# Optimization experiments

Measured on AMD Instinct MI355X. Metric: run time of the kernel, lower is better.

The kernel has to match this reference:

```python
import jax, jax.numpy as jnp
import numpy as np

N = 100000   # nodes
E = 1600000  # edges (avg degree 16)
F_IN, F_HID, F_OUT = 64, 64, 16


def setup_inputs() -> dict:
    key = jax.random.key(0)
    ks = jax.random.split(key, 10)
    features = jax.random.normal(ks[0], (N, F_IN), dtype=jnp.float32)
    src = jax.random.randint(ks[1], (E,), 0, N, dtype=jnp.int32)
    dst = jax.random.randint(ks[2], (E,), 0, N, dtype=jnp.int32)
    # Xavier-uniform weights, zero bias (matches nn.init in the module)
    def xavier(k, fan_in, fan_out):
        lim = np.sqrt(6.0 / (fan_in + fan_out))
        return jax.random.uniform(k, (fan_in, fan_out), jnp.float32, -lim, lim)
    return {
        "features": features,
        "W1": xavier(ks[3], F_IN, F_HID), "b1": jnp.zeros((F_HID,), jnp.float32),
        "W2": xavier(ks[4], F_HID, F_HID), "b2": jnp.zeros((F_HID,), jnp.float32),
        "W3": xavier(ks[5], F_HID, F_OUT), "b3": jnp.zeros((F_OUT,), jnp.float32),
        "src": src, "dst": dst,
    }


def pairnorm_scs(x):
    # PairNorm 'PN-SCS', scale=1
    col_mean = x.mean(axis=0)                                    # [F]
    rownorm = jnp.sqrt(1e-6 + jnp.sum(x * x, axis=1, keepdims=True))  # [N,1]
    return x / rownorm - col_mean


def graph_conv(h, src, dst, W, b):
    # copy_u('h','m') + sum reduce over edges, plus self-loop
    agg = jax.ops.segment_sum(h[src], dst, num_segments=N) + h   # [N,F]
    return agg @ W + b


def reference(features, W1, b1, W2, b2, W3, b3, src, dst):
    h = features
    for W, b in ((W1, b1), (W2, b2)):
        h = pairnorm_scs(h)
        h = jax.nn.relu(graph_conv(h, src, dst, W, b))
        # dropout p=0.0 -> identity
    return graph_conv(h, src, dst, W3, b3)
```

## Files before the change

### kernel.cpp

```cpp
#include <hip/hip_runtime.h>


#define NHB 128

__device__ __forceinline__ unsigned short f2bf(float f) {
  unsigned u = __builtin_bit_cast(unsigned, f);
  u += 0x7FFFu + ((u >> 16) & 1u);
  return (unsigned short)(u >> 16);
}
__device__ __forceinline__ float bf2f(unsigned short h) {
  return __builtin_bit_cast(float, ((unsigned)h) << 16);
}
__device__ __forceinline__ float rlane(float v, int k) {
  return __builtin_bit_cast(
      float, __builtin_amdgcn_readlane(__builtin_bit_cast(int, v), k));
}

__global__ __launch_bounds__(256) void prelude_kernel(
    const int* __restrict__ dst, int* __restrict__ cntA, int E,
    const float* __restrict__ x, float* __restrict__ cs, int n4) {
  __shared__ int lc[NHB];
  __shared__ float lds[16][64];
  const int t = threadIdx.x;
  if (t < NHB) lc[t] = 0;
  __syncthreads();
  const int stride = gridDim.x * blockDim.x;
  for (int e = blockIdx.x * blockDim.x + t; e < E; e += stride)
    atomicAdd(&lc[__builtin_nontemporal_load(&dst[e]) >> 10], 1);

  float s0 = 0.f, s1 = 0.f, s2 = 0.f, s3 = 0.f;
  for (int i = blockIdx.x * blockDim.x + t; i < n4; i += stride) {
    float4 v = ((const float4*)x)[i];
    s0 += v.x; s1 += v.y; s2 += v.z; s3 += v.w;
  }
  const int r = t >> 4;
  const int cq = (t & 15) * 4;
  lds[r][cq + 0] = s0; lds[r][cq + 1] = s1; lds[r][cq + 2] = s2; lds[r][cq + 3] = s3;
  __syncthreads();
  if (t < NHB && lc[t]) atomicAdd(&cntA[t], lc[t]);
  if (t < 64) {
    float tot = 0.f;
    #pragma unroll
    for (int rr = 0; rr < 16; ++rr) tot += lds[rr][t];
    unsafeAtomicAdd(&cs[t], tot);
  }
}

__global__ void colsum_kernel(const float* __restrict__ x, float* __restrict__ cs,
                              int n4) {
  __shared__ float lds[16][64];
  float s0 = 0.f, s1 = 0.f, s2 = 0.f, s3 = 0.f;
  const int t = threadIdx.x;
  const int stride = gridDim.x * blockDim.x;
  for (int i = blockIdx.x * blockDim.x + t; i < n4; i += stride) {
    float4 v = ((const float4*)x)[i];
    s0 += v.x; s1 += v.y; s2 += v.z; s3 += v.w;
  }
  const int r = t >> 4;
  const int cq = (t & 15) * 4;
  lds[r][cq + 0] = s0; lds[r][cq + 1] = s1; lds[r][cq + 2] = s2; lds[r][cq + 3] = s3;
  __syncthreads();
  if (t < 64) {
    float tot = 0.f;
    #pragma unroll
    for (int rr = 0; rr < 16; ++rr) tot += lds[rr][t];
    unsafeAtomicAdd(&cs[t], tot);
  }
}

__global__ __launch_bounds__(256) void matnorm_kernel(
    const float* x, const float* __restrict__ W,
    const float* __restrict__ cs, unsigned short* __restrict__ z,
    int N, float invN) {
  const int lane = threadIdx.x & 63;
  const int wid  = blockIdx.x * (blockDim.x >> 6) + (threadIdx.x >> 6);
  const int nw   = gridDim.x * (blockDim.x >> 6);

  float w[64];
  float cm0 = 0.f, cm1 = 0.f, cm2 = 0.f, cm3 = 0.f;
  #pragma unroll
  for (int k = 0; k < 64; k += 4) {
    w[k + 0] = W[(k + 0) * 64 + lane];
    w[k + 1] = W[(k + 1) * 64 + lane];
    w[k + 2] = W[(k + 2) * 64 + lane];
    w[k + 3] = W[(k + 3) * 64 + lane];
    cm0 = fmaf(cs[k + 0], w[k + 0], cm0);
    cm1 = fmaf(cs[k + 1], w[k + 1], cm1);
    cm2 = fmaf(cs[k + 2], w[k + 2], cm2);
    cm3 = fmaf(cs[k + 3], w[k + 3], cm3);
  }
  const float cm = ((cm0 + cm1) + (cm2 + cm3)) * invN;

  for (int row = wid; row < N; row += nw) {
    const float xv = x[(size_t)row * 64 + lane];
    float ss = xv * xv;
    #pragma unroll
    for (int m = 1; m < 64; m <<= 1) ss += __shfl_xor(ss, m, 64);
    const float rinv = 1.0f / sqrtf(1e-6f + ss);
    float a0 = 0.f, a1 = 0.f, a2 = 0.f, a3 = 0.f;
    #pragma unroll
    for (int k = 0; k < 64; k += 4) {
      a0 = fmaf(rlane(xv, k + 0), w[k + 0], a0);
      a1 = fmaf(rlane(xv, k + 1), w[k + 1], a1);
      a2 = fmaf(rlane(xv, k + 2), w[k + 2], a2);
      a3 = fmaf(rlane(xv, k + 3), w[k + 3], a3);
    }
    const float acc = (a0 + a1) + (a2 + a3);
    z[(size_t)row * 64 + lane] = f2bf(acc * rinv - cm);
  }
}


__global__ void scanA_kernel(const int* __restrict__ cntA,
                             int* __restrict__ baseA, int* __restrict__ curA,
                             int NHI) {
  if (threadIdx.x == 0) {
    int acc = 0;
    for (int p = 0; p < NHI; ++p) { baseA[p] = acc; curA[p] = acc; acc += cntA[p]; }
    baseA[NHI] = acc;
  }
}

#define TILE 2048
#define CAPA 48
__global__ __launch_bounds__(256) void scatterA_kernel(
    const int* __restrict__ src, const int* __restrict__ dst,
    int* __restrict__ curA, unsigned* __restrict__ ppack, int E) {
  __shared__ unsigned lpk[NHB][CAPA];
  __shared__ int lcnt[NHB], lbase[NHB];
  const int t = threadIdx.x;
  if (t < NHB) lcnt[t] = 0;
  __syncthreads();
  const int ntiles = (E + TILE - 1) / TILE;
  for (int tile = blockIdx.x; tile < ntiles; tile += gridDim.x) {
    const int base = tile * TILE;
    #pragma unroll
    for (int j = 0; j < TILE / 256; ++j) {
      const int e = base + j * 256 + t;
      if (e < E) {
        const int d = __builtin_nontemporal_load(&dst[e]);
        const int s = __builtin_nontemporal_load(&src[e]);
        const unsigned pw = ((unsigned)s << 10) | ((unsigned)d & 1023u);
        const int p = d >> 10;
        const int slot = atomicAdd(&lcnt[p], 1);
        if (slot < CAPA) lpk[p][slot] = pw;
        else ppack[atomicAdd(&curA[p], 1)] = pw;
      }
    }
    __syncthreads();
    if (t < NHB) {
      int c = lcnt[t]; if (c > CAPA) c = CAPA;
      lbase[t] = c ? atomicAdd(&curA[t], c) : 0;
      lcnt[t] = c;
    }
    __syncthreads();
    for (int p = 0; p < NHB; ++p) {
      const int c = lcnt[p];
      if (t < c) ppack[lbase[p] + t] = lpk[p][t];
    }
    __syncthreads();
    if (t < NHB) lcnt[t] = 0;
    __syncthreads();
  }
}

__global__ __launch_bounds__(1024) void fillsort_kernel(
    const unsigned* __restrict__ ppack, const int* __restrict__ baseA,
    int* __restrict__ rowstart, int* __restrict__ csr, int N, int E) {
  __shared__ int hist[1024];
  __shared__ int bs[1024];
  const int t = threadIdx.x;
  const int h = blockIdx.x;
  const int nlo = h << 10;
  const int elo = baseA[h], ehi = baseA[h + 1];

  hist[t] = 0;
  __syncthreads();

  int e = elo + t;
  for (; e + 3 * 1024 < ehi; e += 4 * 1024) {
    const unsigned p0 = ppack[e], p1 = ppack[e + 1024],
                   p2 = ppack[e + 2048], p3 = ppack[e + 3072];
    atomicAdd(&hist[p0 & 1023u], 1); atomicAdd(&hist[p1 & 1023u], 1);
    atomicAdd(&hist[p2 & 1023u], 1); atomicAdd(&hist[p3 & 1023u], 1);
  }
  for (; e < ehi; e += 1024) atomicAdd(&hist[ppack[e] & 1023u], 1);
  __syncthreads();

  const int c = hist[t];
  bs[t] = c;
  __syncthreads();
  for (int off = 1; off < 1024; off <<= 1) {
    const int v = (t >= off) ? bs[t - off] : 0;
    __syncthreads();
    bs[t] += v;
    __syncthreads();
  }
  const int excl = bs[t] - c;

  hist[t] = excl;
  const int n0 = nlo + t;
  if (n0 < N) rowstart[n0] = elo + excl;
  if (h == 0 && t == 0) rowstart[N] = E;
  __syncthreads();

  e = elo + t;
  for (; e + 3 * 1024 < ehi; e += 4 * 1024) {
    const unsigned p0 = ppack[e],        p1 = ppack[e + 1024];
    const unsigned p2 = ppack[e + 2048], p3 = ppack[e + 3072];
    csr[elo + atomicAdd(&hist[p0 & 1023u], 1)] = (int)(p0 >> 10);
    csr[elo + atomicAdd(&hist[p1 & 1023u], 1)] = (int)(p1 >> 10);
    csr[elo + atomicAdd(&hist[p2 & 1023u], 1)] = (int)(p2 >> 10);
    csr[elo + atomicAdd(&hist[p3 & 1023u], 1)] = (int)(p3 >> 10);
  }
  for (; e < ehi; e += 1024) {
    const unsigned p = ppack[e];
    csr[elo + atomicAdd(&hist[p & 1023u], 1)] = (int)(p >> 10);
  }
}

__global__ __launch_bounds__(256) void gather64_kernel(
    const unsigned short* __restrict__ z, const float* __restrict__ b,
    const int* __restrict__ rowstart, const int* __restrict__ csr,
    float* __restrict__ agg, int N) {
  const int lane = threadIdx.x & 63;
  int node = blockIdx.x * (blockDim.x >> 6) + (threadIdx.x >> 6);
  if (node >= N) return;
  node = __builtin_amdgcn_readfirstlane(node);
  const int start = rowstart[node];
  const int end   = rowstart[node + 1];
  const unsigned short hs = z[(size_t)node * 64 + lane];
  float a0 = 0.f, a1 = 0.f, a2 = 0.f, a3 = 0.f;
  int e = start;
  for (; e + 16 <= end; e += 16) {
    unsigned short h[16];
    #pragma unroll
    for (int j = 0; j < 16; ++j) h[j] = z[(size_t)csr[e + j] * 64 + lane];
    #pragma unroll
    for (int j = 0; j < 16; j += 4) {
      a0 += bf2f(h[j + 0]); a1 += bf2f(h[j + 1]);
      a2 += bf2f(h[j + 2]); a3 += bf2f(h[j + 3]);
    }
  }
  for (; e + 4 <= end; e += 4) {
    unsigned short h[4];
    #pragma unroll
    for (int j = 0; j < 4; ++j) h[j] = z[(size_t)csr[e + j] * 64 + lane];
    a0 += bf2f(h[0]); a1 += bf2f(h[1]); a2 += bf2f(h[2]); a3 += bf2f(h[3]);
  }
  for (; e < end; ++e) a0 += bf2f(z[(size_t)csr[e] * 64 + lane]);
  const float sum = (a0 + a1) + (a2 + a3);
  agg[(size_t)node * 64 + lane] = fmaxf(bf2f(hs) + b[lane] + sum, 0.f);
}

__global__ __launch_bounds__(256) void gather_l2_kernel(
    const unsigned short* __restrict__ z2, const float* __restrict__ b2,
    const float* __restrict__ W3, const int* __restrict__ rowstart,
    const int* __restrict__ csr, unsigned short* __restrict__ z3, int N) {
  const int lane = threadIdx.x & 63;
  int node = blockIdx.x * (blockDim.x >> 6) + (threadIdx.x >> 6);
  if (node >= N) return;
  node = __builtin_amdgcn_readfirstlane(node);
  float4 w4[4];
  #pragma unroll
  for (int q = 0; q < 4; ++q)
    w4[q] = ((const float4*)(W3 + lane * 16))[q];

  const int start = rowstart[node];
  const int end   = rowstart[node + 1];
  const unsigned short hs = z2[(size_t)node * 64 + lane];
  float a0 = 0.f, a1 = 0.f, a2 = 0.f, a3 = 0.f;
  int e = start;
  for (; e + 16 <= end; e += 16) {
    unsigned short h[16];
    #pragma unroll
    for (int j = 0; j < 16; ++j) h[j] = z2[(size_t)csr[e + j] * 64 + lane];
    #pragma unroll
    for (int j = 0; j < 16; j += 4) {
      a0 += bf2f(h[j + 0]); a1 += bf2f(h[j + 1]);
      a2 += bf2f(h[j + 2]); a3 += bf2f(h[j + 3]);
    }
  }
  for (; e + 4 <= end; e += 4) {
    unsigned short h[4];
    #pragma unroll
    for (int j = 0; j < 4; ++j) h[j] = z2[(size_t)csr[e + j] * 64 + lane];
    a0 += bf2f(h[0]); a1 += bf2f(h[1]); a2 += bf2f(h[2]); a3 += bf2f(h[3]);
  }
  for (; e < end; ++e) a0 += bf2f(z2[(size_t)csr[e] * 64 + lane]);
  const float sum = (a0 + a1) + (a2 + a3);
  const float o = fmaxf(bf2f(hs) + b2[lane] + sum, 0.f);

  float p[16];
  #pragma unroll
  for (int q = 0; q < 4; ++q) {
    p[4 * q + 0] = o * w4[q].x;
    p[4 * q + 1] = o * w4[q].y;
    p[4 * q + 2] = o * w4[q].z;
    p[4 * q + 3] = o * w4[q].w;
  }
  {
    const bool up = (lane & 1);
    #pragma unroll
    for (int m = 0; m < 8; ++m) {
      const float mine = up ? p[m + 8] : p[m];
      const float give = up ? p[m] : p[m + 8];
      p[m] = mine + __shfl_xor(give, 1, 64);
    }
  }
  {
    const bool up = (lane & 2);
    #pragma unroll
    for (int m = 0; m < 4; ++m) {
      const float mine = up ? p[m + 4] : p[m];
      const float give = up ? p[m] : p[m + 4];
      p[m] = mine + __shfl_xor(give, 2, 64);
    }
  }
  {
    const bool up = (lane & 4);
    #pragma unroll
    for (int m = 0; m < 2; ++m) {
      const float mine = up ? p[m + 2] : p[m];
      const float give = up ? p[m] : p[m + 2];
      p[m] = mine + __shfl_xor(give, 4, 64);
    }
  }
  {
    const bool up = (lane & 8);
    const float mine = up ? p[1] : p[0];
    const float give = up ? p[0] : p[1];
    p[0] = mine + __shfl_xor(give, 8, 64);
  }
  p[0] += __shfl_xor(p[0], 16, 64);
  p[0] += __shfl_xor(p[0], 32, 64);

  if (lane < 16) {
    const int j = ((lane & 1) << 3) | ((lane & 2) << 1) |
                  ((lane & 4) >> 1) | ((lane & 8) >> 3);
    z3[(size_t)node * 16 + j] = f2bf(p[0]);
  }
}

__global__ __launch_bounds__(256) void gather16_kernel(
    const unsigned short* __restrict__ z3, const float* __restrict__ b3,
    const int* __restrict__ rowstart, const int* __restrict__ csr,
    float* __restrict__ out, int N) {
  const int lane = threadIdx.x & 63;
  const int f = lane & 15;
  const int g = lane >> 4;
  int node = blockIdx.x * (blockDim.x >> 6) + (threadIdx.x >> 6);
  if (node >= N) return;
  node = __builtin_amdgcn_readfirstlane(node);
  const int start = rowstart[node];
  const int end   = rowstart[node + 1];
  float acc0 = 0.f, acc1 = 0.f;
  int e = start + g;
  for (; e + 4 < end; e += 8) {
    acc0 += bf2f(z3[(size_t)csr[e] * 16 + f]);
    acc1 += bf2f(z3[(size_t)csr[e + 4] * 16 + f]);
  }
  if (e < end) acc0 += bf2f(z3[(size_t)csr[e] * 16 + f]);
  float acc = acc0 + acc1;
  acc += __shfl_xor(acc, 16, 64);
  acc += __shfl_xor(acc, 32, 64);
  if (lane < 16)
    out[(size_t)node * 16 + f] = bf2f(z3[(size_t)node * 16 + f]) + b3[f] + acc;
}

extern "C" void kernel_launch(void* const* d_in, const int* in_sizes, int n_in,
                              void* d_out, int out_size, void* d_ws, size_t ws_size,
                              hipStream_t stream) {
  const float* feat = (const float*)d_in[0];
  const float* W1 = (const float*)d_in[1];
  const float* b1 = (const float*)d_in[2];
  const float* W2 = (const float*)d_in[3];
  const float* b2 = (const float*)d_in[4];
  const float* W3 = (const float*)d_in[5];
  const float* b3 = (const float*)d_in[6];
  const int* src = (const int*)d_in[7];
  const int* dst = (const int*)d_in[8];
  const int N = in_sizes[0] / 64;
  const int E = in_sizes[7];
  float* out = (float*)d_out;

  float* B            = (float*)d_ws;
  unsigned short* zb  = (unsigned short*)(B + (size_t)N * 64);
  unsigned short* z3b = zb + (size_t)N * 64;
  int* cntA  = (int*)(z3b + (size_t)N * 16);
  float* cs1 = (float*)(cntA + NHB);
  float* cs2 = cs1 + 64;
  int* baseA    = (int*)(cs2 + 64);
  int* curA     = baseA + NHB + 1;
  int* rowstart = curA + NHB;
  int* csr      = rowstart + N + 1;
  unsigned* ppack = (unsigned*)zb;

  const int NHI = (N + 1023) >> 10;
  const int node_blocks = (N + 3) / 4;
  const float invN = 1.0f / (float)N;

  hipMemsetAsync(cntA, 0, (NHB + 128) * sizeof(int), stream);
  prelude_kernel<<<512, 256, 0, stream>>>(dst, cntA, E, feat, cs1, N * 16);
  scanA_kernel<<<1, 64, 0, stream>>>(cntA, baseA, curA, NHI);
  scatterA_kernel<<<512, 256, 0, stream>>>(src, dst, curA, ppack, E);
  fillsort_kernel<<<NHI, 1024, 0, stream>>>(ppack, baseA, rowstart, csr, N, E);

  matnorm_kernel<<<1024, 256, 0, stream>>>(feat, W1, cs1, zb, N, invN);
  gather64_kernel<<<node_blocks, 256, 0, stream>>>(zb, b1, rowstart, csr, B, N);

  colsum_kernel<<<512, 256, 0, stream>>>(B, cs2, N * 16);
  matnorm_kernel<<<1024, 256, 0, stream>>>(B, W2, cs2, zb, N, invN);
  gather_l2_kernel<<<node_blocks, 256, 0, stream>>>(zb, b2, W3, rowstart, csr,
                                                    z3b, N);

  gather16_kernel<<<node_blocks, 256, 0, stream>>>(z3b, b3, rowstart, csr, out, N);
}
```

Before: 402.5 us.

## Process two nodes per wavefront in 64-wide gathers with shuffled CSR indices

The two 64-feature gather kernels now give each wavefront a pair of adjacent nodes instead of one. The combined neighbor index list (up to 64 entries) is loaded once with a single coalesced read and broadcast with shuffles, replacing per-edge scalar index loads. Neighbor rows are fetched in full batches of 16 across the node boundary to keep more loads in flight. Extra branching and per-edge tails handle the split point, and the grid is halved, which may reduce the number of waves available to hide latency.

```diff
diff --git a/kernel.cpp b/kernel.cpp
--- a/kernel.cpp
+++ b/kernel.cpp
@@ -224,73 +224,68 @@
     const int* __restrict__ rowstart, const int* __restrict__ csr,
     float* __restrict__ agg, int N) {
   const int lane = threadIdx.x & 63;
-  int node = blockIdx.x * (blockDim.x >> 6) + (threadIdx.x >> 6);
-  if (node >= N) return;
-  node = __builtin_amdgcn_readfirstlane(node);
-  const int start = rowstart[node];
-  const int end   = rowstart[node + 1];
-  const unsigned short hs = z[(size_t)node * 64 + lane];
-  float a0 = 0.f, a1 = 0.f, a2 = 0.f, a3 = 0.f;
-  int e = start;
-  for (; e + 16 <= end; e += 16) {
+  int pair = blockIdx.x * (blockDim.x >> 6) + (threadIdx.x >> 6);
+  const int n0 = pair << 1;
+  if (n0 >= N) return;
+  pair = __builtin_amdgcn_readfirstlane(pair);
+  const int has2 = (n0 + 1 < N);
+  const int s0  = rowstart[n0];
+  const int mid = rowstart[n0 + 1];
+  const int e1  = has2 ? rowstart[n0 + 2] : mid;
+  const int ntot = e1 - s0;
+  const int nA   = mid - s0;
+
+  const int cidx = (lane < ntot) ? csr[s0 + lane] : 0;
+
+  const unsigned short hs0 = z[(size_t)n0 * 64 + lane];
+  const unsigned short hs1 = has2 ? z[(size_t)(n0 + 1) * 64 + lane] : (unsigned short)0;
+
+  float aA0 = 0.f, aA1 = 0.f, aA2 = 0.f, aA3 = 0.f;
+  float aB0 = 0.f, aB1 = 0.f, aB2 = 0.f, aB3 = 0.f;
+  const int lim = ntot < 64 ? ntot : 64;
+  for (int j0 = 0; j0 < lim; j0 += 16) {
+    int id[16];
+    #pragma unroll
+    for (int k = 0; k < 16; ++k) id[k] = __shfl(cidx, j0 + k, 64);
     unsigned short h[16];
     #pragma unroll
-    for (int j = 0; j < 16; ++j) h[j] = z[(size_t)csr[e + j] * 64 + lane];
-    #pragma unroll
-    for (int j = 0; j < 16; j += 4) {
-      a0 += bf2f(h[j + 0]); a1 += bf2f(h[j + 1]);
-      a2 += bf2f(h[j + 2]); a3 += bf2f(h[j + 3]);
-    }
-  }
-  for (; e + 4 <= end; e += 4) {
-    unsigned short h[4];
-    #pragma unroll
-    for (int j = 0; j < 4; ++j) h[j] = z[(size_t)csr[e + j] * 64 + lane];
-    a0 += bf2f(h[0]); a1 += bf2f(h[1]); a2 += bf2f(h[2]); a3 += bf2f(h[3]);
-  }
-  for (; e < end; ++e) a0 += bf2f(z[(size_t)csr[e] * 64 + lane]);
-  const float sum = (a0 + a1) + (a2 + a3);
-  agg[(size_t)node * 64 + lane] = fmaxf(bf2f(hs) + b[lane] + sum, 0.f);
-}
-
-__global__ __launch_bounds__(256) void gather_l2_kernel(
-    const unsigned short* __restrict__ z2, const float* __restrict__ b2,
-    const float* __restrict__ W3, const int* __restrict__ rowstart,
-    const int* __restrict__ csr, unsigned short* __restrict__ z3, int N) {
-  const int lane = threadIdx.x & 63;
-  int node = blockIdx.x * (blockDim.x >> 6) + (threadIdx.x >> 6);
-  if (node >= N) return;
-  node = __builtin_amdgcn_readfirstlane(node);
-  float4 w4[4];
-  #pragma unroll
-  for (int q = 0; q < 4; ++q)
-    w4[q] = ((const float4*)(W3 + lane * 16))[q];
-
-  const int start = rowstart[node];
-  const int end   = rowstart[node + 1];
-  const unsigned short hs = z2[(size_t)node * 64 + lane];
-  float a0 = 0.f, a1 = 0.f, a2 = 0.f, a3 = 0.f;
-  int e = start;
-  for (; e + 16 <= end; e += 16) {
-    unsigned short h[16];
-    #pragma unroll
-    for (int j = 0; j < 16; ++j) h[j] = z2[(size_t)csr[e + j] * 64 + lane];
-    #pragma unroll
-    for (int j = 0; j < 16; j += 4) {
-      a0 += bf2f(h[j + 0]); a1 += bf2f(h[j + 1]);
-      a2 += bf2f(h[j + 2]); a3 += bf2f(h[j + 3]);
-    }
-  }
-  for (; e + 4 <= end; e += 4) {
-    unsigned short h[4];
-    #pragma unroll
-    for (int j = 0; j < 4; ++j) h[j] = z2[(size_t)csr[e + j] * 64 + lane];
-    a0 += bf2f(h[0]); a1 += bf2f(h[1]); a2 += bf2f(h[2]); a3 += bf2f(h[3]);
-  }
-  for (; e < end; ++e) a0 += bf2f(z2[(size_t)csr[e] * 64 + lane]);
-  const float sum = (a0 + a1) + (a2 + a3);
-  const float o = fmaxf(bf2f(hs) + b2[lane] + sum, 0.f);
-
+    for (int k = 0; k < 16; ++k) h[k] = z[(size_t)id[k] * 64 + lane];
+    if (j0 + 16 <= nA) {
+      #pragma unroll
+      for (int k = 0; k < 16; k += 4) {
+        aA0 += bf2f(h[k + 0]); aA1 += bf2f(h[k + 1]);
+        aA2 += bf2f(h[k + 2]); aA3 += bf2f(h[k + 3]);
+      }
+    } else if (j0 >= nA && j0 + 16 <= lim) {
+      #pragma unroll
+      for (int k = 0; k < 16; k += 4) {
+        aB0 += bf2f(h[k + 0]); aB1 += bf2f(h[k + 1]);
+        aB2 += bf2f(h[k + 2]); aB3 += bf2f(h[k + 3]);
+      }
+    } else {
+      #pragma unroll
+      for (int k = 0; k < 16; ++k) {
+        const int j = j0 + k;
+        const float v = (j < lim) ? bf2f(h[k]) : 0.f;
+        if (j < nA) aA0 += v; else aB0 += v;
+      }
+    }
+  }
+  for (int e = s0 + 64; e < e1; ++e) {
+    const float v = bf2f(z[(size_t)csr[e] * 64 + lane]);
+    if (e < mid) aA0 += v; else aB0 += v;
+  }
+
+  const float sumA = (aA0 + aA1) + (aA2 + aA3);
+  agg[(size_t)n0 * 64 + lane] = fmaxf(bf2f(hs0) + b[lane] + sumA, 0.f);
+  if (has2) {
+    const float sumB = (aB0 + aB1) + (aB2 + aB3);
+    agg[(size_t)(n0 + 1) * 64 + lane] = fmaxf(bf2f(hs1) + b[lane] + sumB, 0.f);
+  }
+}
+
+__device__ __forceinline__ void w3_matvec_store(
+    float o, const float4* w4, int lane, unsigned short* __restrict__ z3row) {
   float p[16];
   #pragma unroll
   for (int q = 0; q < 4; ++q) {
@@ -334,11 +329,82 @@
   }
   p[0] += __shfl_xor(p[0], 16, 64);
   p[0] += __shfl_xor(p[0], 32, 64);
-
   if (lane < 16) {
     const int j = ((lane & 1) << 3) | ((lane & 2) << 1) |
                   ((lane & 4) >> 1) | ((lane & 8) >> 3);
-    z3[(size_t)node * 16 + j] = f2bf(p[0]);
+    z3row[j] = f2bf(p[0]);
+  }
+}
+
+__global__ __launch_bounds__(256) void gather_l2_kernel(
+    const unsigned short* __restrict__ z2, const float* __restrict__ b2,
+    const float* __restrict__ W3, const int* __restrict__ rowstart,
+    const int* __restrict__ csr, unsigned short* __restrict__ z3, int N) {
+  const int lane = threadIdx.x & 63;
+  int pair = blockIdx.x * (blockDim.x >> 6) + (threadIdx.x >> 6);
+  const int n0 = pair << 1;
+  if (n0 >= N) return;
+  pair = __builtin_amdgcn_readfirstlane(pair);
+  float4 w4[4];
+  #pragma unroll
+  for (int q = 0; q < 4; ++q)
+    w4[q] = ((const float4*)(W3 + lane * 16))[q];
+
+  const int has2 = (n0 + 1 < N);
+  const int s0  = rowstart[n0];
+  const int mid = rowstart[n0 + 1];
+  const int e1  = has2 ? rowstart[n0 + 2] : mid;
+  const int ntot = e1 - s0;
+  const int nA   = mid - s0;
+
+  const int cidx = (lane < ntot) ? csr[s0 + lane] : 0;
+
+  const unsigned short hs0 = z2[(size_t)n0 * 64 + lane];
+  const unsigned short hs1 = has2 ? z2[(size_t)(n0 + 1) * 64 + lane] : (unsigned short)0;
+
+  float aA0 = 0.f, aA1 = 0.f, aA2 = 0.f, aA3 = 0.f;
+  float aB0 = 0.f, aB1 = 0.f, aB2 = 0.f, aB3 = 0.f;
+  const int lim = ntot < 64 ? ntot : 64;
+  for (int j0 = 0; j0 < lim; j0 += 16) {
+    int id[16];
+    #pragma unroll
+    for (int k = 0; k < 16; ++k) id[k] = __shfl(cidx, j0 + k, 64);
+    unsigned short h[16];
+    #pragma unroll
+    for (int k = 0; k < 16; ++k) h[k] = z2[(size_t)id[k] * 64 + lane];
+    if (j0 + 16 <= nA) {
+      #pragma unroll
+      for (int k = 0; k < 16; k += 4) {
+        aA0 += bf2f(h[k + 0]); aA1 += bf2f(h[k + 1]);
+        aA2 += bf2f(h[k + 2]); aA3 += bf2f(h[k + 3]);
+      }
+    } else if (j0 >= nA && j0 + 16 <= lim) {
+      #pragma unroll
+      for (int k = 0; k < 16; k += 4) {
+        aB0 += bf2f(h[k + 0]); aB1 += bf2f(h[k + 1]);
+        aB2 += bf2f(h[k + 2]); aB3 += bf2f(h[k + 3]);
+      }
+    } else {
+      #pragma unroll
+      for (int k = 0; k < 16; ++k) {
+        const int j = j0 + k;
+        const float v = (j < lim) ? bf2f(h[k]) : 0.f;
+        if (j < nA) aA0 += v; else aB0 += v;
+      }
+    }
+  }
+  for (int e = s0 + 64; e < e1; ++e) {
+    const float v = bf2f(z2[(size_t)csr[e] * 64 + lane]);
+    if (e < mid) aA0 += v; else aB0 += v;
+  }
+
+  const float sumA = (aA0 + aA1) + (aA2 + aA3);
+  const float oA = fmaxf(bf2f(hs0) + b2[lane] + sumA, 0.f);
+  w3_matvec_store(oA, w4, lane, z3 + (size_t)n0 * 16);
+  if (has2) {
+    const float sumB = (aB0 + aB1) + (aB2 + aB3);
+    const float oB = fmaxf(bf2f(hs1) + b2[lane] + sumB, 0.f);
+    w3_matvec_store(oB, w4, lane, z3 + (size_t)(n0 + 1) * 16);
   }
 }
 
@@ -398,6 +464,8 @@
 
   const int NHI = (N + 1023) >> 10;
   const int node_blocks = (N + 3) / 4;
+  const int npairs = (N + 1) / 2;
+  const int pair_blocks = (npairs + 3) / 4;
   const float invN = 1.0f / (float)N;
 
   hipMemsetAsync(cntA, 0, (NHB + 128) * sizeof(int), stream);
@@ -407,11 +475,11 @@
   fillsort_kernel<<<NHI, 1024, 0, stream>>>(ppack, baseA, rowstart, csr, N, E);
 
   matnorm_kernel<<<1024, 256, 0, stream>>>(feat, W1, cs1, zb, N, invN);
-  gather64_kernel<<<node_blocks, 256, 0, stream>>>(zb, b1, rowstart, csr, B, N);
+  gather64_kernel<<<pair_blocks, 256, 0, stream>>>(zb, b1, rowstart, csr, B, N);
 
   colsum_kernel<<<512, 256, 0, stream>>>(B, cs2, N * 16);
   matnorm_kernel<<<1024, 256, 0, stream>>>(B, W2, cs2, zb, N, invN);
-  gather_l2_kernel<<<node_blocks, 256, 0, stream>>>(zb, b2, W3, rowstart, csr,
+  gather_l2_kernel<<<pair_blocks, 256, 0, stream>>>(zb, b2, W3, rowstart, csr,
                                                     z3b, N);
 
   gather16_kernel<<<node_blocks, 256, 0, stream>>>(z3b, b3, rowstart, csr, out, N);
```

Measured after the change: 403.9 us. About the same (+0.3%).
